# Kernel optimization log

Hardware: AMD Instinct MI355X
Metric: run time of the kernel (lower is better)

Reference implementation:

```python
import jax, jax.numpy as jnp
import numpy as np

N_NODES = 100000
N_EDGES = 1600000


def setup_inputs() -> dict:
    key = jax.random.key(0)
    k1, k2, k3, k4 = jax.random.split(key, 4)
    x = jax.random.normal(k1, (N_NODES, 16), dtype=jnp.float32)
    edge_index = jax.random.randint(k2, (2, N_EDGES), 0, N_NODES, dtype=jnp.int32)
    # Glorot-ish init for the two GCN layers
    W1 = jax.random.normal(k3, (16, 32), dtype=jnp.float32) * (1.0 / np.sqrt(16))
    b1 = jnp.zeros((32,), dtype=jnp.float32)
    W2 = jax.random.normal(k4, (32, 2), dtype=jnp.float32) * (1.0 / np.sqrt(32))
    b2 = jnp.zeros((2,), dtype=jnp.float32)
    return {"x": x, "edge_index": edge_index, "W1": W1, "b1": b1, "W2": W2, "b2": b2}


def _gcn_conv(x, W, b, src, dst, norm, n_nodes):
    # PyG GCNConv: h = X @ W; aggregate norm * h[src] at dst; add bias.
    h = x @ W                                   # [N, out]
    msg = h[src] * norm[:, None]                # [E+N, out] gather + scale
    out = jax.ops.segment_sum(msg, dst, num_segments=n_nodes)
    return out + b


def reference(x, edge_index, W1, b1, W2, b2):
    n = x.shape[0]
    self_loops = jnp.arange(n, dtype=edge_index.dtype)
    src = jnp.concatenate([edge_index[0], self_loops])  # [E+N]
    dst = jnp.concatenate([edge_index[1], self_loops])
    # Symmetric GCN normalization: deg computed on graph with self-loops
    deg = jax.ops.segment_sum(jnp.ones_like(dst, dtype=x.dtype), dst, num_segments=n)
    dis = jnp.where(deg > 0, jax.lax.rsqrt(deg), 0.0)   # deg^{-1/2}
    norm = dis[src] * dis[dst]                          # [E+N]

    h = jax.nn.relu(_gcn_conv(x, W1, b1, src, dst, norm, n))
    out = _gcn_conv(h, W2, b2, src, dst, norm, n)
    return out
```

## Files before the change

kernel.cpp:

```cpp
#include <hip/hip_runtime.h>
#include <hip/hip_fp16.h>

static constexpr int N  = 100000;
static constexpr int E  = 1600000;
static constexpr int B  = 256;

static constexpr int BC     = 1024;
static constexpr int CHUNKC = 6144;
static constexpr int PERC   = CHUNKC / BC;
static constexpr int NBLKC  = (E + CHUNKC - 1) / CHUNKC;
static constexpr int NBUCK  = (N + 127) / 128;
static constexpr int SLAB   = 3072;
static constexpr int GCS    = 16;


__global__ __launch_bounds__(BC) void kC_scatter(
        const int* __restrict__ src, const int* __restrict__ dst,
        int* __restrict__ gcur, int* __restrict__ gslab) {
    __shared__ int lhist[NBUCK];
    __shared__ int lbase[NBUCK];
    __shared__ int gb[NBUCK];
    __shared__ int wsum[16];
    __shared__ int stage[CHUNKC];

    int t = threadIdx.x, blk = blockIdx.x;
    for (int i = t; i < NBUCK; i += BC) lhist[i] = 0;
    __syncthreads();

    int eb = blk * CHUNKC;
    int ns = min(CHUNKC, E - eb);
    int ds[PERC], ss[PERC];
#pragma unroll
    for (int k = 0; k < PERC; ++k) {
        int idx = k * BC + t;
        if (idx < ns) {
            ds[k] = dst[eb + idx];
            ss[k] = src[eb + idx];
            atomicAdd(&lhist[ds[k] >> 7], 1);
        }
    }
    __syncthreads();

    int lane = t & 63, wv = t >> 6;
    int val = (t < NBUCK) ? lhist[t] : 0;
    int inc = val;
#pragma unroll
    for (int off = 1; off < 64; off <<= 1) {
        int u = __shfl_up(inc, off, 64);
        if (lane >= off) inc += u;
    }
    if (lane == 63) wsum[wv] = inc;
    __syncthreads();
    if (wv == 0) {
        int wval = (lane < 16) ? wsum[lane] : 0;
        int winc = wval;
#pragma unroll
        for (int off = 1; off < 16; off <<= 1) {
            int u = __shfl_up(winc, off, 64);
            if (lane >= off) winc += u;
        }
        if (lane < 16) wsum[lane] = winc - wval;
    }
    __syncthreads();
    if (t < NBUCK) lbase[t] = wsum[wv] + inc - val;

    __syncthreads();
    if (t < NBUCK) {
        int h = lhist[t];
        if (h > 0) gb[t] = t * SLAB + atomicAdd(&gcur[t * GCS], h);
        lhist[t] = 0;
    }
    __syncthreads();

#pragma unroll
    for (int k = 0; k < PERC; ++k) {
        int idx = k * BC + t;
        if (idx < ns) {
            int d = ds[k], b = d >> 7;
            int r = atomicAdd(&lhist[b], 1);
            stage[lbase[b] + r] = ss[k] | ((d & 127) << 17);
        }
    }
    __syncthreads();

    for (int slot = t; slot < ns; slot += BC) {
        int b = 0;
        for (int step = 512; step; step >>= 1) {
            int nb = b + step;
            if (nb < NBUCK && lbase[nb] <= slot) b = nb;
        }
        int idx = gb[b] + (slot - lbase[b]);
        if (idx < (b + 1) * SLAB) gslab[idx] = stage[slot];
    }
}


__global__ void kD1_deg(const int* __restrict__ gcur, const int* __restrict__ gslab,
                        int* __restrict__ rofs, const float4* __restrict__ x4,
                        __half* __restrict__ xpre) {
    __shared__ int c[128];
    __shared__ int wq[2];
    int t = threadIdx.x, b = blockIdx.x;
    if (t < 128) c[t] = 0;
    __syncthreads();

    int ne = min(gcur[b * GCS], SLAB);
    int base = b * SLAB;
    for (int k = t; k < ne; k += B)
        atomicAdd(&c[gslab[base + k] >> 17], 1);
    __syncthreads();

    int lane = t & 63, wv = t >> 6;
    int val = (t < 128) ? c[t] : 0;
    int inc = val;
#pragma unroll
    for (int off = 1; off < 64; off <<= 1) {
        int u = __shfl_up(inc, off, 64);
        if (lane >= off) inc += u;
    }
    if (t == 63) wq[0] = inc;
    __syncthreads();
    if (t < 128) rofs[b * 129 + t] = base + inc - val + ((wv == 1) ? wq[0] : 0);
    if (t == 128) rofs[b * 129 + 128] = base + ne;

    int n = b * 128 + (t >> 1), h = t & 1;
    if (n < N) {
        float d = rsqrtf((float)(c[t >> 1] + 1));
        float4 u0 = x4[(size_t)n * 4 + h * 2];
        float4 u1 = x4[(size_t)n * 4 + h * 2 + 1];
        ushort4 p0, p1;
        p0.x = __half_as_ushort(__float2half(u0.x * d));
        p0.y = __half_as_ushort(__float2half(u0.y * d));
        p0.z = __half_as_ushort(__float2half(u0.z * d));
        p0.w = __half_as_ushort(__float2half(u0.w * d));
        p1.x = __half_as_ushort(__float2half(u1.x * d));
        p1.y = __half_as_ushort(__float2half(u1.y * d));
        p1.z = __half_as_ushort(__float2half(u1.z * d));
        p1.w = __half_as_ushort(__float2half(u1.w * d));
        *(ushort4*)(xpre + (size_t)n * 16 + h * 8)     = p0;
        *(ushort4*)(xpre + (size_t)n * 16 + h * 8 + 4) = p1;
    }
}


__global__ __launch_bounds__(B) void kD2_agg(
        const __half* __restrict__ xpre, int* __restrict__ gslab,
        const int* __restrict__ rofs, const float* __restrict__ W1,
        const float* __restrict__ b1, const float* __restrict__ W2,
        float2* __restrict__ hpre) {
    __shared__ int st1[SLAB];
    __shared__ int cur[128];
    __shared__ int lofs[129];
    __shared__ float acc[128 * 17];
    __shared__ float sW1[512], sb1[32], sW2[64];
    int t = threadIdx.x, b = blockIdx.x;
    for (int i = t; i < 512; i += B) sW1[i] = W1[i];
    if (t < 32) sb1[t] = b1[t];
    if (t < 64) sW2[t] = W2[t];
    if (t < 128) cur[t] = 0;
    int base = b * SLAB;
    if (t < 129) lofs[t] = rofs[b * 129 + t] - base;
    __syncthreads();

    int ne = lofs[128];
    for (int k = t; k < ne; k += B) {
        int p = gslab[base + k];
        int lo = p >> 17;
        int r = atomicAdd(&cur[lo], 1);
        st1[lofs[lo] + r] = p & 0x1FFFF;
    }
    __syncthreads();
    for (int k = t; k < ne; k += B) gslab[base + k] = st1[k];

    int nl = t >> 1, h = t & 1;
    int n = b * 128 + nl;
    if (n < N) {
        int rs = lofs[nl], re = lofs[nl + 1];
        float a0, a1, a2, a3, a4, a5, a6, a7;
        {
            int4 w = *(const int4*)(xpre + (size_t)n * 16 + h * 8);
            float2 q0 = __half22float2(*(__half2*)&w.x);
            float2 q1 = __half22float2(*(__half2*)&w.y);
            float2 q2 = __half22float2(*(__half2*)&w.z);
            float2 q3 = __half22float2(*(__half2*)&w.w);
            a0 = q0.x; a1 = q0.y; a2 = q1.x; a3 = q1.y;
            a4 = q2.x; a5 = q2.y; a6 = q3.x; a7 = q3.y;
        }
        auto add8 = [&](int4 w) {
            float2 q0 = __half22float2(*(__half2*)&w.x);
            float2 q1 = __half22float2(*(__half2*)&w.y);
            float2 q2 = __half22float2(*(__half2*)&w.z);
            float2 q3 = __half22float2(*(__half2*)&w.w);
            a0 += q0.x; a1 += q0.y; a2 += q1.x; a3 += q1.y;
            a4 += q2.x; a5 += q2.y; a6 += q3.x; a7 += q3.y;
        };
        int k = rs;
        for (; k + 4 <= re; k += 4) {
            int s0 = st1[k], s1 = st1[k + 1], s2 = st1[k + 2], s3 = st1[k + 3];
            int4 v0 = *(const int4*)(xpre + (size_t)s0 * 16 + h * 8);
            int4 v1 = *(const int4*)(xpre + (size_t)s1 * 16 + h * 8);
            int4 v2 = *(const int4*)(xpre + (size_t)s2 * 16 + h * 8);
            int4 v3 = *(const int4*)(xpre + (size_t)s3 * 16 + h * 8);
            add8(v0); add8(v1); add8(v2); add8(v3);
        }
        for (; k < re; ++k)
            add8(*(const int4*)(xpre + (size_t)st1[k] * 16 + h * 8));
        float* row = acc + nl * 17 + h * 8;
        row[0] = a0; row[1] = a1; row[2] = a2; row[3] = a3;
        row[4] = a4; row[5] = a5; row[6] = a6; row[7] = a7;
    }
    __syncthreads();

    if (t < 128) {
        int n2 = b * 128 + t;
        if (n2 < N) {
            int deg = lofs[t + 1] - lofs[t];
            float d = rsqrtf((float)(deg + 1));
            const float* row = acc + t * 17;
            float xi[16];
#pragma unroll
            for (int k = 0; k < 16; ++k) xi[k] = row[k] * d;
            float o0 = 0.f, o1 = 0.f;
#pragma unroll
            for (int c = 0; c < 32; ++c) {
                float hh = sb1[c];
#pragma unroll
                for (int k = 0; k < 16; ++k) hh = fmaf(xi[k], sW1[k * 32 + c], hh);
                hh = fmaxf(hh, 0.f);
                o0 = fmaf(hh, sW2[c * 2 + 0], o0);
                o1 = fmaf(hh, sW2[c * 2 + 1], o1);
            }
            hpre[n2] = make_float2(d * o0, d * o1);
        }
    }
}


__global__ void kF_l2(const float2* __restrict__ hpre, const int* __restrict__ gslab,
                      const int* __restrict__ rofs, const float* __restrict__ b2,
                      float2* __restrict__ out) {
    int n = blockIdx.x * B + threadIdx.x;
    if (n >= N) return;
    int bb = n >> 7, lo = n & 127;
    int rs = rofs[bb * 129 + lo], re = rofs[bb * 129 + lo + 1];
    float2 self = hpre[n];
    float o0 = self.x, o1 = self.y;
    int k = rs;
    for (; k + 4 <= re; k += 4) {
        int s0 = gslab[k], s1 = gslab[k + 1], s2 = gslab[k + 2], s3 = gslab[k + 3];
        float2 v0 = hpre[s0];
        float2 v1 = hpre[s1];
        float2 v2 = hpre[s2];
        float2 v3 = hpre[s3];
        o0 += (v0.x + v1.x) + (v2.x + v3.x);
        o1 += (v0.y + v1.y) + (v2.y + v3.y);
    }
    for (; k < re; ++k) {
        float2 v = hpre[gslab[k]];
        o0 += v.x; o1 += v.y;
    }
    float d = rsqrtf((float)(re - rs + 1));
    out[n] = make_float2(fmaf(d, o0, b2[0]), fmaf(d, o1, b2[1]));
}


extern "C" void kernel_launch(void* const* d_in, const int* in_sizes, int n_in,
                              void* d_out, int out_size, void* d_ws, size_t ws_size,
                              hipStream_t stream) {
    const float* x  = (const float*)d_in[0];
    const int*   ei = (const int*)d_in[1];
    const float* W1 = (const float*)d_in[2];
    const float* b1 = (const float*)d_in[3];
    const float* W2 = (const float*)d_in[4];
    const float* b2 = (const float*)d_in[5];

    const int* src = ei;
    const int* dst = ei + E;

    int*    gslab = (int*)d_ws;
    int*    rofs  = gslab + (size_t)NBUCK * SLAB;
    int*    gcur  = rofs + 100880;
    float*  hpre  = (float*)(gcur + 12512);
    __half* xpre  = (__half*)(hpre + 2 * (size_t)N);

    hipMemsetAsync(gcur, 0, NBUCK * GCS * sizeof(int), stream);
    kC_scatter<<<NBLKC, BC, 0, stream>>>(src, dst, gcur, gslab);
    kD1_deg<<<NBUCK, B, 0, stream>>>(gcur, gslab, rofs, (const float4*)x, xpre);
    kD2_agg<<<NBUCK, B, 0, stream>>>(xpre, gslab, rofs, W1, b1, W2, (float2*)hpre);
    kF_l2<<<(N + B - 1) / B, B, 0, stream>>>((const float2*)hpre, gslab, rofs, b2,
                                             (float2*)d_out);
}
```

Baseline: 132.1 us.

## Split per-node gathers across more threads and rebalance scatter kernel grid

The edge scatter kernel now runs 512 blocks of 512 threads with 3125 edges each, so each thread scans two buckets in the prefix sum. The layer-1 aggregation kernel doubles its block to 512 threads and gives each node four threads: two split the feature halves and two split the edges, combined with a shuffle. The layer-2 kernel likewise uses two threads per node over interleaved edges. The degree histogram reads slab entries as int4. The goal is more memory-level parallelism in the gather loops, paid for with extra shuffles and lower per-thread work.

```diff
diff --git a/kernel.cpp b/kernel.cpp
--- a/kernel.cpp
+++ b/kernel.cpp
@@ -5,13 +5,14 @@
 static constexpr int E  = 1600000;
 static constexpr int B  = 256;
 
-static constexpr int BC     = 1024;
-static constexpr int CHUNKC = 6144;
-static constexpr int PERC   = CHUNKC / BC;
-static constexpr int NBLKC  = (E + CHUNKC - 1) / CHUNKC;
+static constexpr int BC     = 512;
+static constexpr int CHUNKC = 3125;
+static constexpr int PERC   = 7;
+static constexpr int NBLKC  = 512;
 static constexpr int NBUCK  = (N + 127) / 128;
 static constexpr int SLAB   = 3072;
 static constexpr int GCS    = 16;
+static constexpr int B2     = 512;
 
 
 __global__ __launch_bounds__(BC) void kC_scatter(
@@ -20,7 +21,7 @@
     __shared__ int lhist[NBUCK];
     __shared__ int lbase[NBUCK];
     __shared__ int gb[NBUCK];
-    __shared__ int wsum[16];
+    __shared__ int wsum[8];
     __shared__ int stage[CHUNKC];
 
     int t = threadIdx.x, blk = blockIdx.x;
@@ -42,8 +43,11 @@
     __syncthreads();
 
     int lane = t & 63, wv = t >> 6;
-    int val = (t < NBUCK) ? lhist[t] : 0;
-    int inc = val;
+    int i0 = 2 * t;
+    int v0 = (i0 < NBUCK) ? lhist[i0] : 0;
+    int v1 = (i0 + 1 < NBUCK) ? lhist[i0 + 1] : 0;
+    int sum = v0 + v1;
+    int inc = sum;
 #pragma unroll
     for (int off = 1; off < 64; off <<= 1) {
         int u = __shfl_up(inc, off, 64);
@@ -52,23 +56,27 @@
     if (lane == 63) wsum[wv] = inc;
     __syncthreads();
     if (wv == 0) {
-        int wval = (lane < 16) ? wsum[lane] : 0;
+        int wval = (lane < 8) ? wsum[lane] : 0;
         int winc = wval;
 #pragma unroll
-        for (int off = 1; off < 16; off <<= 1) {
+        for (int off = 1; off < 8; off <<= 1) {
             int u = __shfl_up(winc, off, 64);
             if (lane >= off) winc += u;
         }
-        if (lane < 16) wsum[lane] = winc - wval;
-    }
-    __syncthreads();
-    if (t < NBUCK) lbase[t] = wsum[wv] + inc - val;
-
-    __syncthreads();
-    if (t < NBUCK) {
-        int h = lhist[t];
-        if (h > 0) gb[t] = t * SLAB + atomicAdd(&gcur[t * GCS], h);
-        lhist[t] = 0;
+        if (lane < 8) wsum[lane] = winc - wval;
+    }
+    __syncthreads();
+    {
+        int ex = wsum[wv] + inc - sum;
+        if (i0 < NBUCK) lbase[i0] = ex;
+        if (i0 + 1 < NBUCK) lbase[i0 + 1] = ex + v0;
+    }
+    __syncthreads();
+
+    for (int bb = t; bb < NBUCK; bb += BC) {
+        int h = lhist[bb];
+        if (h > 0) gb[bb] = bb * SLAB + atomicAdd(&gcur[bb * GCS], h);
+        lhist[bb] = 0;
     }
     __syncthreads();
 
@@ -106,8 +114,15 @@
 
     int ne = min(gcur[b * GCS], SLAB);
     int base = b * SLAB;
-    for (int k = t; k < ne; k += B)
-        atomicAdd(&c[gslab[base + k] >> 17], 1);
+    int ne4 = ne & ~3;
+    for (int k = 4 * t; k < ne4; k += 4 * B) {
+        int4 p4 = *(const int4*)(gslab + base + k);
+        atomicAdd(&c[p4.x >> 17], 1);
+        atomicAdd(&c[p4.y >> 17], 1);
+        atomicAdd(&c[p4.z >> 17], 1);
+        atomicAdd(&c[p4.w >> 17], 1);
+    }
+    if (t < ne - ne4) atomicAdd(&c[gslab[base + ne4 + t] >> 17], 1);
     __syncthreads();
 
     int lane = t & 63, wv = t >> 6;
@@ -143,7 +158,7 @@
 }
 
 
-__global__ __launch_bounds__(B) void kD2_agg(
+__global__ __launch_bounds__(B2) void kD2_agg(
         const __half* __restrict__ xpre, int* __restrict__ gslab,
         const int* __restrict__ rofs, const float* __restrict__ W1,
         const float* __restrict__ b1, const float* __restrict__ W2,
@@ -154,7 +169,7 @@
     __shared__ float acc[128 * 17];
     __shared__ float sW1[512], sb1[32], sW2[64];
     int t = threadIdx.x, b = blockIdx.x;
-    for (int i = t; i < 512; i += B) sW1[i] = W1[i];
+    if (t < 512) sW1[t] = W1[t];
     if (t < 32) sb1[t] = b1[t];
     if (t < 64) sW2[t] = W2[t];
     if (t < 128) cur[t] = 0;
@@ -163,51 +178,60 @@
     __syncthreads();
 
     int ne = lofs[128];
-    for (int k = t; k < ne; k += B) {
+    for (int k = t; k < ne; k += B2) {
         int p = gslab[base + k];
         int lo = p >> 17;
         int r = atomicAdd(&cur[lo], 1);
         st1[lofs[lo] + r] = p & 0x1FFFF;
     }
     __syncthreads();
-    for (int k = t; k < ne; k += B) gslab[base + k] = st1[k];
-
-    int nl = t >> 1, h = t & 1;
+    for (int k = t; k < ne; k += B2) gslab[base + k] = st1[k];
+
+    int nl = t >> 2, h = t & 1, eh = (t >> 1) & 1;
     int n = b * 128 + nl;
-    if (n < N) {
-        int rs = lofs[nl], re = lofs[nl + 1];
-        float a0, a1, a2, a3, a4, a5, a6, a7;
-        {
-            int4 w = *(const int4*)(xpre + (size_t)n * 16 + h * 8);
-            float2 q0 = __half22float2(*(__half2*)&w.x);
-            float2 q1 = __half22float2(*(__half2*)&w.y);
-            float2 q2 = __half22float2(*(__half2*)&w.z);
-            float2 q3 = __half22float2(*(__half2*)&w.w);
-            a0 = q0.x; a1 = q0.y; a2 = q1.x; a3 = q1.y;
-            a4 = q2.x; a5 = q2.y; a6 = q3.x; a7 = q3.y;
-        }
-        auto add8 = [&](int4 w) {
-            float2 q0 = __half22float2(*(__half2*)&w.x);
-            float2 q1 = __half22float2(*(__half2*)&w.y);
-            float2 q2 = __half22float2(*(__half2*)&w.z);
-            float2 q3 = __half22float2(*(__half2*)&w.w);
-            a0 += q0.x; a1 += q0.y; a2 += q1.x; a3 += q1.y;
-            a4 += q2.x; a5 += q2.y; a6 += q3.x; a7 += q3.y;
-        };
-        int k = rs;
-        for (; k + 4 <= re; k += 4) {
-            int s0 = st1[k], s1 = st1[k + 1], s2 = st1[k + 2], s3 = st1[k + 3];
-            int4 v0 = *(const int4*)(xpre + (size_t)s0 * 16 + h * 8);
-            int4 v1 = *(const int4*)(xpre + (size_t)s1 * 16 + h * 8);
-            int4 v2 = *(const int4*)(xpre + (size_t)s2 * 16 + h * 8);
-            int4 v3 = *(const int4*)(xpre + (size_t)s3 * 16 + h * 8);
-            add8(v0); add8(v1); add8(v2); add8(v3);
-        }
-        for (; k < re; ++k)
-            add8(*(const int4*)(xpre + (size_t)st1[k] * 16 + h * 8));
-        float* row = acc + nl * 17 + h * 8;
-        row[0] = a0; row[1] = a1; row[2] = a2; row[3] = a3;
-        row[4] = a4; row[5] = a5; row[6] = a6; row[7] = a7;
+    {
+        float a0 = 0.f, a1 = 0.f, a2 = 0.f, a3 = 0.f;
+        float a4 = 0.f, a5 = 0.f, a6 = 0.f, a7 = 0.f;
+        if (n < N) {
+            int rs = lofs[nl], re = lofs[nl + 1];
+            if (eh == 0) {
+                int4 w = *(const int4*)(xpre + (size_t)n * 16 + h * 8);
+                float2 q0 = __half22float2(*(__half2*)&w.x);
+                float2 q1 = __half22float2(*(__half2*)&w.y);
+                float2 q2 = __half22float2(*(__half2*)&w.z);
+                float2 q3 = __half22float2(*(__half2*)&w.w);
+                a0 = q0.x; a1 = q0.y; a2 = q1.x; a3 = q1.y;
+                a4 = q2.x; a5 = q2.y; a6 = q3.x; a7 = q3.y;
+            }
+            auto add8 = [&](int4 w) {
+                float2 q0 = __half22float2(*(__half2*)&w.x);
+                float2 q1 = __half22float2(*(__half2*)&w.y);
+                float2 q2 = __half22float2(*(__half2*)&w.z);
+                float2 q3 = __half22float2(*(__half2*)&w.w);
+                a0 += q0.x; a1 += q0.y; a2 += q1.x; a3 += q1.y;
+                a4 += q2.x; a5 += q2.y; a6 += q3.x; a7 += q3.y;
+            };
+            int k = rs + eh;
+            for (; k + 6 < re; k += 8) {
+                int s0 = st1[k], s1 = st1[k + 2], s2 = st1[k + 4], s3 = st1[k + 6];
+                int4 v0 = *(const int4*)(xpre + (size_t)s0 * 16 + h * 8);
+                int4 v1 = *(const int4*)(xpre + (size_t)s1 * 16 + h * 8);
+                int4 v2 = *(const int4*)(xpre + (size_t)s2 * 16 + h * 8);
+                int4 v3 = *(const int4*)(xpre + (size_t)s3 * 16 + h * 8);
+                add8(v0); add8(v1); add8(v2); add8(v3);
+            }
+            for (; k < re; k += 2)
+                add8(*(const int4*)(xpre + (size_t)st1[k] * 16 + h * 8));
+        }
+        a0 += __shfl_xor(a0, 2, 64); a1 += __shfl_xor(a1, 2, 64);
+        a2 += __shfl_xor(a2, 2, 64); a3 += __shfl_xor(a3, 2, 64);
+        a4 += __shfl_xor(a4, 2, 64); a5 += __shfl_xor(a5, 2, 64);
+        a6 += __shfl_xor(a6, 2, 64); a7 += __shfl_xor(a7, 2, 64);
+        if (n < N && eh == 0) {
+            float* row = acc + nl * 17 + h * 8;
+            row[0] = a0; row[1] = a1; row[2] = a2; row[3] = a3;
+            row[4] = a4; row[5] = a5; row[6] = a6; row[7] = a7;
+        }
     }
     __syncthreads();
 
@@ -239,28 +263,38 @@
 __global__ void kF_l2(const float2* __restrict__ hpre, const int* __restrict__ gslab,
                       const int* __restrict__ rofs, const float* __restrict__ b2,
                       float2* __restrict__ out) {
-    int n = blockIdx.x * B + threadIdx.x;
-    if (n >= N) return;
-    int bb = n >> 7, lo = n & 127;
-    int rs = rofs[bb * 129 + lo], re = rofs[bb * 129 + lo + 1];
-    float2 self = hpre[n];
-    float o0 = self.x, o1 = self.y;
-    int k = rs;
-    for (; k + 4 <= re; k += 4) {
-        int s0 = gslab[k], s1 = gslab[k + 1], s2 = gslab[k + 2], s3 = gslab[k + 3];
-        float2 v0 = hpre[s0];
-        float2 v1 = hpre[s1];
-        float2 v2 = hpre[s2];
-        float2 v3 = hpre[s3];
-        o0 += (v0.x + v1.x) + (v2.x + v3.x);
-        o1 += (v0.y + v1.y) + (v2.y + v3.y);
-    }
-    for (; k < re; ++k) {
-        float2 v = hpre[gslab[k]];
-        o0 += v.x; o1 += v.y;
-    }
-    float d = rsqrtf((float)(re - rs + 1));
-    out[n] = make_float2(fmaf(d, o0, b2[0]), fmaf(d, o1, b2[1]));
+    int g = blockIdx.x * B + threadIdx.x;
+    int n = g >> 1, eh = g & 1;
+    float o0 = 0.f, o1 = 0.f;
+    if (n < N) {
+        int bb = n >> 7, lo = n & 127;
+        int rs = rofs[bb * 129 + lo], re = rofs[bb * 129 + lo + 1];
+        if (eh == 0) {
+            float2 self = hpre[n];
+            o0 = self.x; o1 = self.y;
+        }
+        int k = rs + eh;
+        for (; k + 6 < re; k += 8) {
+            int s0 = gslab[k], s1 = gslab[k + 2], s2 = gslab[k + 4], s3 = gslab[k + 6];
+            float2 v0 = hpre[s0];
+            float2 v1 = hpre[s1];
+            float2 v2 = hpre[s2];
+            float2 v3 = hpre[s3];
+            o0 += (v0.x + v1.x) + (v2.x + v3.x);
+            o1 += (v0.y + v1.y) + (v2.y + v3.y);
+        }
+        for (; k < re; k += 2) {
+            float2 v = hpre[gslab[k]];
+            o0 += v.x; o1 += v.y;
+        }
+    }
+    o0 += __shfl_xor(o0, 1, 64);
+    o1 += __shfl_xor(o1, 1, 64);
+    if (n < N && eh == 0) {
+        int bb = n >> 7, lo = n & 127;
+        float d = rsqrtf((float)(rofs[bb * 129 + lo + 1] - rofs[bb * 129 + lo] + 1));
+        out[n] = make_float2(fmaf(d, o0, b2[0]), fmaf(d, o1, b2[1]));
+    }
 }
 
 
@@ -286,7 +320,7 @@
     hipMemsetAsync(gcur, 0, NBUCK * GCS * sizeof(int), stream);
     kC_scatter<<<NBLKC, BC, 0, stream>>>(src, dst, gcur, gslab);
     kD1_deg<<<NBUCK, B, 0, stream>>>(gcur, gslab, rofs, (const float4*)x, xpre);
-    kD2_agg<<<NBUCK, B, 0, stream>>>(xpre, gslab, rofs, W1, b1, W2, (float2*)hpre);
-    kF_l2<<<(N + B - 1) / B, B, 0, stream>>>((const float2*)hpre, gslab, rofs, b2,
-                                             (float2*)d_out);
-}
+    kD2_agg<<<NBUCK, B2, 0, stream>>>(xpre, gslab, rofs, W1, b1, W2, (float2*)hpre);
+    kF_l2<<<(2 * N + B - 1) / B, B, 0, stream>>>((const float2*)hpre, gslab, rofs, b2,
+                                                 (float2*)d_out);
+}
```

Result: slower. 141.7 us (+7.2%).

## Resize scatter chunks, copy buckets per-thread, vectorize degree-count slab reads

Applied to the files above, without the earlier changes.

The edge chunk per block changes so that exactly 256 blocks cover all edges, which removes the tail bound check. The final stage-to-global write drops the per-slot binary search over bucket offsets. Instead, one thread per bucket copies that bucket's contiguous run serially. The degree kernel reads slab entries as int4 vectors. Together these cut instruction overhead, at the cost of less coalesced stores and uneven per-thread work in the copy loop.

```diff
diff --git a/kernel.cpp b/kernel.cpp
--- a/kernel.cpp
+++ b/kernel.cpp
@@ -6,9 +6,9 @@
 static constexpr int B  = 256;
 
 static constexpr int BC     = 1024;
-static constexpr int CHUNKC = 6144;
-static constexpr int PERC   = CHUNKC / BC;
-static constexpr int NBLKC  = (E + CHUNKC - 1) / CHUNKC;
+static constexpr int NBLKC  = 256;
+static constexpr int CHUNKC = E / NBLKC;
+static constexpr int PERC   = (CHUNKC + BC - 1) / BC;
 static constexpr int NBUCK  = (N + 127) / 128;
 static constexpr int SLAB   = 3072;
 static constexpr int GCS    = 16;
@@ -28,12 +28,11 @@
     __syncthreads();
 
     int eb = blk * CHUNKC;
-    int ns = min(CHUNKC, E - eb);
     int ds[PERC], ss[PERC];
 #pragma unroll
     for (int k = 0; k < PERC; ++k) {
         int idx = k * BC + t;
-        if (idx < ns) {
+        if (idx < CHUNKC) {
             ds[k] = dst[eb + idx];
             ss[k] = src[eb + idx];
             atomicAdd(&lhist[ds[k] >> 7], 1);
@@ -63,8 +62,8 @@
     }
     __syncthreads();
     if (t < NBUCK) lbase[t] = wsum[wv] + inc - val;
-
-    __syncthreads();
+    __syncthreads();
+
     if (t < NBUCK) {
         int h = lhist[t];
         if (h > 0) gb[t] = t * SLAB + atomicAdd(&gcur[t * GCS], h);
@@ -75,7 +74,7 @@
 #pragma unroll
     for (int k = 0; k < PERC; ++k) {
         int idx = k * BC + t;
-        if (idx < ns) {
+        if (idx < CHUNKC) {
             int d = ds[k], b = d >> 7;
             int r = atomicAdd(&lhist[b], 1);
             stage[lbase[b] + r] = ss[k] | ((d & 127) << 17);
@@ -83,14 +82,16 @@
     }
     __syncthreads();
 
-    for (int slot = t; slot < ns; slot += BC) {
-        int b = 0;
-        for (int step = 512; step; step >>= 1) {
-            int nb = b + step;
-            if (nb < NBUCK && lbase[nb] <= slot) b = nb;
-        }
-        int idx = gb[b] + (slot - lbase[b]);
-        if (idx < (b + 1) * SLAB) gslab[idx] = stage[slot];
+    if (t < NBUCK) {
+        int len = lhist[t];
+        if (len > 0) {
+            int s0 = lbase[t];
+            int g  = gb[t];
+            int cap = (t + 1) * SLAB - g;
+            if (cap < 0) cap = 0;
+            if (len > cap) len = cap;
+            for (int i = 0; i < len; ++i) gslab[g + i] = stage[s0 + i];
+        }
     }
 }
 
@@ -106,8 +107,15 @@
 
     int ne = min(gcur[b * GCS], SLAB);
     int base = b * SLAB;
-    for (int k = t; k < ne; k += B)
-        atomicAdd(&c[gslab[base + k] >> 17], 1);
+    int ne4 = ne & ~3;
+    for (int k = 4 * t; k < ne4; k += 4 * B) {
+        int4 p4 = *(const int4*)(gslab + base + k);
+        atomicAdd(&c[p4.x >> 17], 1);
+        atomicAdd(&c[p4.y >> 17], 1);
+        atomicAdd(&c[p4.z >> 17], 1);
+        atomicAdd(&c[p4.w >> 17], 1);
+    }
+    if (t < ne - ne4) atomicAdd(&c[gslab[base + ne4 + t] >> 17], 1);
     __syncthreads();
 
     int lane = t & 63, wv = t >> 6;
```

Measured after the change: 128.8 us. -2.5%, faster.
